# Kernel optimization log

Hardware: AMD Instinct MI355X
Metric: run time of the kernel (lower is better)

## Reference

```python
import jax, jax.numpy as jnp
import numpy as np

N, E, H, C, NG = 50000, 800000, 4, 64, 32
HC = H * C  # 256


def setup_inputs() -> dict:
    key = jax.random.key(0)
    ks = jax.random.split(key, 32)
    f32 = jnp.float32
    def rn(k, shape, s=0.1):
        return jax.random.normal(k, shape, dtype=f32) * s
    inp = {}
    inp['x'] = jax.random.normal(ks[0], (N, 4), dtype=f32)
    inp['edge_index'] = jax.random.randint(ks[1], (2, E), 0, N, dtype=jnp.int32)
    inp['edge_attr'] = jax.random.normal(ks[2], (E, 1), dtype=f32)
    inp['batch'] = jnp.sort(jax.random.randint(ks[3], (N,), 0, NG, dtype=jnp.int32))
    # encoder
    inp['enc_w'] = rn(ks[4], (4, 64)); inp['enc_b'] = rn(ks[5], (64,))
    # GATv2 layer 1: in 64 -> H*C (lin_l source, lin_r target, lin_edge, att, bias)
    inp['g1_wl'] = rn(ks[6], (64, HC)); inp['g1_bl'] = rn(ks[7], (HC,))
    inp['g1_wr'] = rn(ks[8], (64, HC)); inp['g1_br'] = rn(ks[9], (HC,))
    inp['g1_we'] = rn(ks[10], (1, HC))
    inp['g1_att'] = rn(ks[11], (H, C))
    inp['g1_bias'] = rn(ks[12], (HC,))
    # GATv2 layer 2: in 256 -> H*C
    inp['g2_wl'] = rn(ks[13], (HC, HC)); inp['g2_bl'] = rn(ks[14], (HC,))
    inp['g2_wr'] = rn(ks[15], (HC, HC)); inp['g2_br'] = rn(ks[16], (HC,))
    inp['g2_we'] = rn(ks[17], (1, HC))
    inp['g2_att'] = rn(ks[18], (H, C))
    inp['g2_bias'] = rn(ks[19], (HC,))
    # post MLP: 256 -> 128 (LayerNorm, ReLU) -> 64 (ReLU)
    inp['p1_w'] = rn(ks[20], (HC, 128)); inp['p1_b'] = rn(ks[21], (128,))
    inp['ln_g'] = jnp.ones((128,), dtype=f32); inp['ln_b'] = jnp.zeros((128,), dtype=f32)
    inp['p2_w'] = rn(ks[22], (128, 64)); inp['p2_b'] = rn(ks[23], (64,))
    return inp


def _gatv2_layer(x, src, dst, eattr, wl, bl, wr, br, we, att, bias):
    # PyG GATv2Conv: alpha_e = att . leaky_relu(lin_l(x_src) + lin_r(x_dst) + lin_edge(e))
    n = x.shape[0]
    xl = (x @ wl + bl).reshape(n, H, C)   # source-side messages
    xr = (x @ wr + br).reshape(n, H, C)   # target-side
    e = (eattr @ we).reshape(-1, H, C)
    m = jax.nn.leaky_relu(xl[src] + xr[dst] + e, 0.2)        # [E',H,C]
    alpha = jnp.einsum('ehc,hc->eh', m, att)                  # [E',H]
    amax = jax.lax.stop_gradient(jax.ops.segment_max(alpha, dst, num_segments=n))
    ex = jnp.exp(alpha - amax[dst])
    den = jax.ops.segment_sum(ex, dst, num_segments=n)
    a = ex / den[dst]                                          # softmax per dst node
    out = jax.ops.segment_sum(a[:, :, None] * xl[src], dst, num_segments=n)
    return out.reshape(n, HC) + bias


def reference(x, edge_index, edge_attr, batch, enc_w, enc_b,
              g1_wl, g1_bl, g1_wr, g1_br, g1_we, g1_att, g1_bias,
              g2_wl, g2_bl, g2_wr, g2_br, g2_we, g2_att, g2_bias,
              p1_w, p1_b, ln_g, ln_b, p2_w, p2_b):
    n = x.shape[0]
    src0, dst0 = edge_index[0], edge_index[1]
    # PyG default add_self_loops=True with fill_value='mean' for edge_attr
    deg = jnp.maximum(jax.ops.segment_sum(jnp.ones_like(edge_attr[:, 0]), dst0, num_segments=n), 1.0)
    loop_attr = jax.ops.segment_sum(edge_attr, dst0, num_segments=n) / deg[:, None]
    idx = jnp.arange(n, dtype=src0.dtype)
    src = jnp.concatenate([src0, idx]); dst = jnp.concatenate([dst0, idx])
    eattr = jnp.concatenate([edge_attr, loop_attr], axis=0)
    h = jax.nn.relu(x @ enc_w + enc_b)
    h = jax.nn.relu(_gatv2_layer(h, src, dst, eattr, g1_wl, g1_bl, g1_wr, g1_br, g1_we, g1_att, g1_bias))
    h = jax.nn.relu(_gatv2_layer(h, src, dst, eattr, g2_wl, g2_bl, g2_wr, g2_br, g2_we, g2_att, g2_bias))
    # global mean pool over graphs
    cnt = jnp.maximum(jax.ops.segment_sum(jnp.ones((n,), h.dtype), batch, num_segments=NG), 1.0)
    g = jax.ops.segment_sum(h, batch, num_segments=NG) / cnt[:, None]
    # post MLP (dropout is identity in eval)
    z = g @ p1_w + p1_b
    mu = jnp.mean(z, axis=-1, keepdims=True)
    var = jnp.mean((z - mu) ** 2, axis=-1, keepdims=True)
    z = (z - mu) / jnp.sqrt(var + 1e-5) * ln_g + ln_b
    z = jax.nn.relu(z)
    z = jax.nn.relu(z @ p2_w + p2_b)
    return z
```

## Files before the change

kernel.cpp:

```cpp
#include <hip/hip_runtime.h>

#define CDIV(a,b) (((a)+(b)-1)/(b))

typedef __bf16 bf16_t;
typedef unsigned char u8;
typedef bf16_t bf16x8 __attribute__((ext_vector_type(8)));
typedef float floatx4 __attribute__((ext_vector_type(4)));
typedef float floatx2 __attribute__((ext_vector_type(2)));

__device__ __forceinline__ int sigma2(int p) {
    int tile = p >> 7, hh = (p >> 6) & 1, m = (p >> 2) & 15, c = p & 3;
    return tile * 128 + (hh * 4 + c) * 16 + m;
}

__device__ __forceinline__ unsigned pack4_fp8(float a, float b, float c, float d) {
    int v = __builtin_amdgcn_cvt_pk_fp8_f32(a, b, 0, false);
    v = __builtin_amdgcn_cvt_pk_fp8_f32(c, d, v, true);
    return (unsigned)v;
}

template<bool HI>
__device__ __forceinline__ floatx2 cvtf8(unsigned v) {
    return __builtin_amdgcn_cvt_pk_f32_fp8(v, HI);
}

template<int CTRL>
__device__ __forceinline__ float dpp_add(float x) {
    int v = __builtin_amdgcn_update_dpp(0, __float_as_int(x), CTRL, 0xf, 0xf, true);
    return x + __int_as_float(v);
}

__global__ void k_deg(const int* __restrict__ ei, int* __restrict__ deg, int E) {
    int e = blockIdx.x * 256 + threadIdx.x;
    if (e >= E) return;
    atomicAdd(&deg[ei[E + e]], 1);
}

__global__ void k_histB(const int* __restrict__ deg, int* __restrict__ blockcnt,
                        int n, int nb) {
    __shared__ int h[64];
    int t = threadIdx.x;
    if (t < 64) h[t] = 0;
    __syncthreads();
    int i = blockIdx.x * 256 + t;
    if (i < n) {
        int d = deg[i]; if (d > 63) d = 63;
        atomicAdd(&h[63 - d], 1);
    }
    __syncthreads();
    if (t < 64) blockcnt[t * nb + blockIdx.x] = h[t];
}
__global__ void k_scan2(const int* __restrict__ bc, int* __restrict__ bo, int total) {
    __shared__ int wsum[4];
    __shared__ int carrysh;
    int t = threadIdx.x;
    int w = t >> 6, lane = t & 63;
    if (t == 0) carrysh = 0;
    __syncthreads();
    for (int base = 0; base < total; base += 256) {
        int carry = carrysh;
        int i = base + t;
        int v = (i < total) ? bc[i] : 0;
        int s = v;
        for (int d = 1; d < 64; d <<= 1) {
            int u = __shfl_up(s, d);
            if (lane >= d) s += u;
        }
        if (lane == 63) wsum[w] = s;
        __syncthreads();
        int wadd = 0;
        if (w > 0) wadd += wsum[0];
        if (w > 1) wadd += wsum[1];
        if (w > 2) wadd += wsum[2];
        if (i < total) bo[i] = carry + wadd + s - v;
        __syncthreads();
        if (t == 255) carrysh = carry + wadd + s;
        __syncthreads();
    }
}
__global__ void k_scatter2(const int* __restrict__ deg, const int* __restrict__ bo,
                           int* __restrict__ perm, int n, int nb) {
    __shared__ int h[64];
    int t = threadIdx.x;
    if (t < 64) h[t] = 0;
    __syncthreads();
    int i = blockIdx.x * 256 + t;
    int b = 0, r = 0;
    if (i < n) {
        int d = deg[i]; if (d > 63) d = 63;
        b = 63 - d;
        r = atomicAdd(&h[b], 1);
    }
    __syncthreads();
    if (i < n) perm[bo[b * nb + blockIdx.x] + r] = i;
}

__global__ void k_scanA(const int* __restrict__ deg, int* __restrict__ part, int n) {
    __shared__ int sh[256];
    int t = threadIdx.x;
    int i = blockIdx.x * 256 + t;
    int v = (i < n) ? deg[i] + 1 : 0;
    sh[t] = v;
    __syncthreads();
    for (int d = 128; d > 0; d >>= 1) { if (t < d) sh[t] += sh[t + d]; __syncthreads(); }
    if (t == 0) part[blockIdx.x] = sh[0];
}
__global__ void k_scanB(int* __restrict__ part, int nb) {
    __shared__ int sh[256];
    int t = threadIdx.x;
    int v = (t < nb) ? part[t] : 0;
    sh[t] = v;
    __syncthreads();
    for (int d = 1; d < 256; d <<= 1) {
        int u = (t >= d) ? sh[t - d] : 0;
        __syncthreads();
        sh[t] += u;
        __syncthreads();
    }
    if (t < nb) part[t] = sh[t] - v;
}
__global__ void k_scanC(const int* __restrict__ deg, const int* __restrict__ part,
                        int* __restrict__ off, int n) {
    __shared__ int sh[256];
    int t = threadIdx.x;
    int i = blockIdx.x * 256 + t;
    int v = (i < n) ? deg[i] + 1 : 0;
    sh[t] = v;
    __syncthreads();
    for (int d = 1; d < 256; d <<= 1) {
        int u = (t >= d) ? sh[t - d] : 0;
        __syncthreads();
        sh[t] += u;
        __syncthreads();
    }
    int excl = part[blockIdx.x] + sh[t] - v;
    if (i < n) off[i] = excl;
    if (i == n - 1) off[n] = excl + v;
}

__global__ void k_fill(const int* __restrict__ ei, const float* __restrict__ ea,
                       const int* __restrict__ off, int* __restrict__ cursor,
                       int2* __restrict__ csr, int E) {
    int e = blockIdx.x * 256 + threadIdx.x;
    if (e >= E) return;
    int s = ei[e], d = ei[E + e];
    int pos = off[d] + atomicAdd(&cursor[d], 1);
    csr[pos] = make_int2(s, __float_as_int(ea[e]));
}

__global__ void k_selfloop(const int* __restrict__ off, int2* __restrict__ csr, int n) {
    int i = blockIdx.x * 256 + threadIdx.x;
    if (i >= n) return;
    int p0 = off[i], p1 = off[i + 1] - 1;
    float s = 0.0f;
    for (int p = p0; p < p1; ++p) s += __int_as_float(csr[p].y);
    float la = s / fmaxf((float)(p1 - p0), 1.0f);
    csr[p1] = make_int2(i, __float_as_int(la));
}

__global__ void k_wcast2(const float* __restrict__ Wl, const float* __restrict__ Wr,
                         const float* __restrict__ bl, const float* __restrict__ br,
                         bf16_t* __restrict__ Wt, float* __restrict__ bias2,
                         int K, int kshift, int permK,
                         const float* __restrict__ we, const float* __restrict__ att,
                         const float* __restrict__ cb,
                         float* __restrict__ wep, float* __restrict__ attp,
                         float* __restrict__ cbp) {
    int idx = blockIdx.x * 256 + threadIdx.x;
    if (idx < 512) bias2[idx] = (idx < 256) ? bl[idx] : br[idx - 256];
    if (idx < 256) {
        int sg = sigma2(idx);
        wep[idx] = we[sg]; attp[idx] = att[sg]; cbp[idx] = cb[sg];
    }
    if (idx >= 512 * K) return;
    int nn = idx >> kshift, k = idx & (K - 1);
    int ks = permK ? sigma2(k) : k;
    float v = (nn < 256) ? Wl[ks * 256 + nn] : Wr[ks * 256 + (nn - 256)];
    Wt[idx] = (bf16_t)v;
}

__global__ __launch_bounds__(256) void k_gemm1_fused(
        const float* __restrict__ x, const float* __restrict__ encw,
        const float* __restrict__ encb, const bf16_t* __restrict__ Wt,
        const float* __restrict__ bias2, u8* __restrict__ XL,
        u8* __restrict__ XR, int nrows) {
    __shared__ bf16_t As[128 * 32];
    __shared__ bf16_t Bs[128 * 32];
    int tid = threadIdx.x;
    int w = tid >> 6, lane = tid & 63;
    int quad = lane >> 4, m = lane & 15;
    int row0 = blockIdx.x * 128;
    int ct0 = blockIdx.y * 2;
    bf16x8 afr[2][2];
    floatx4 acc[2][8];

    for (int ctile = ct0; ctile < ct0 + 2; ++ctile) {
        int n0 = ctile * 128;
#pragma unroll
        for (int rt = 0; rt < 2; ++rt)
#pragma unroll
            for (int ct = 0; ct < 8; ++ct)
                acc[rt][ct] = (floatx4){0.f, 0.f, 0.f, 0.f};
        for (int k0c = 0; k0c < 2; ++k0c) {
            __syncthreads();
            if (ctile == ct0) {
#pragma unroll
                for (int i = 0; i < 2; ++i) {
                    int c = tid + i * 256;
                    int r = c >> 2, kc = c & 3;
                    int sw = (kc + (r >> 1)) & 3;
                    int gr = row0 + r; if (gr >= nrows) gr = nrows - 1;
                    float4 xv = ((const float4*)x)[gr];
                    bf16x8 v;
#pragma unroll
                    for (int kk = 0; kk < 8; ++kk) {
                        int k = k0c * 32 + kc * 8 + kk;
                        float s = encb[k];
                        s = fmaf(xv.x, encw[k], s);
                        s = fmaf(xv.y, encw[64 + k], s);
                        s = fmaf(xv.z, encw[128 + k], s);
                        s = fmaf(xv.w, encw[192 + k], s);
                        v[kk] = (bf16_t)fmaxf(s, 0.0f);
                    }
                    *(bf16x8*)&As[r * 32 + sw * 8] = v;
                }
            }
#pragma unroll
            for (int i = 0; i < 2; ++i) {
                int c = tid + i * 256;
                int r = c >> 2, kc = c & 3;
                int sw = (kc + (r >> 1)) & 3;
                bf16x8 v = *(const bf16x8*)&Wt[(size_t)(n0 + r) * 64 + k0c * 32 + kc * 8];
                *(bf16x8*)&Bs[r * 32 + sw * 8] = v;
            }
            __syncthreads();
            if (ctile == ct0) {
#pragma unroll
                for (int rt = 0; rt < 2; ++rt) {
                    int ar = w * 32 + rt * 16 + m;
                    afr[k0c][rt] = *(bf16x8*)&As[ar * 32 + (((quad + (ar >> 1)) & 3) * 8)];
                }
            }
            bf16x8 bfr[8];
#pragma unroll
            for (int ct = 0; ct < 8; ++ct) {
                int br = ct * 16 + m;
                bfr[ct] = *(bf16x8*)&Bs[br * 32 + (((quad + (br >> 1)) & 3) * 8)];
            }
#pragma unroll
            for (int ct = 0; ct < 8; ++ct) {
                acc[0][ct] = __builtin_amdgcn_mfma_f32_16x16x32_bf16(afr[k0c][0], bfr[ct], acc[0][ct], 0, 0, 0);
                acc[1][ct] = __builtin_amdgcn_mfma_f32_16x16x32_bf16(afr[k0c][1], bfr[ct], acc[1][ct], 0, 0, 0);
            }
        }
        int tile = ctile & 1;
        u8* dst = (ctile < 2) ? XL : XR;
        float bv[8];
#pragma unroll
        for (int ct = 0; ct < 8; ++ct) bv[ct] = bias2[n0 + ct * 16 + m];
#pragma unroll
        for (int rt = 0; rt < 2; ++rt) {
#pragma unroll
            for (int i = 0; i < 4; ++i) {
                int row = row0 + w * 32 + rt * 16 + quad * 4 + i;
                if (row < nrows) {
                    unsigned w0 = pack4_fp8(acc[rt][0][i] + bv[0], acc[rt][1][i] + bv[1],
                                            acc[rt][2][i] + bv[2], acc[rt][3][i] + bv[3]);
                    unsigned w1 = pack4_fp8(acc[rt][4][i] + bv[4], acc[rt][5][i] + bv[5],
                                            acc[rt][6][i] + bv[6], acc[rt][7][i] + bv[7]);
                    *(unsigned*)&dst[(size_t)row * 256 + tile * 128 + m * 4] = w0;
                    *(unsigned*)&dst[(size_t)row * 256 + tile * 128 + 64 + m * 4] = w1;
                }
            }
        }
    }
}

__global__ __launch_bounds__(256) void k_gemm2(
        const bf16_t* __restrict__ Hb, const bf16_t* __restrict__ Wt,
        const float* __restrict__ bias2, u8* __restrict__ XL,
        u8* __restrict__ XR, int nrows) {
    const int K = 256;
    __shared__ bf16_t As[128 * 32];
    __shared__ bf16_t Bs[128 * 32];
    int tid = threadIdx.x;
    int w = tid >> 6, lane = tid & 63;
    int quad = lane >> 4, m = lane & 15;
    int row0 = blockIdx.x * 128;
    int ct0 = blockIdx.y * 2;
    bf16x8 afr[8][2];
    floatx4 acc[2][8];

    for (int ctile = ct0; ctile < ct0 + 2; ++ctile) {
        int n0 = ctile * 128;
#pragma unroll
        for (int rt = 0; rt < 2; ++rt)
#pragma unroll
            for (int ct = 0; ct < 8; ++ct)
                acc[rt][ct] = (floatx4){0.f, 0.f, 0.f, 0.f};
        for (int k0c = 0; k0c < 8; ++k0c) {
            __syncthreads();
            if (ctile == ct0) {
#pragma unroll
                for (int i = 0; i < 2; ++i) {
                    int c = tid + i * 256;
                    int r = c >> 2, kc = c & 3;
                    int sw = (kc + (r >> 1)) & 3;
                    int gr = row0 + r; if (gr >= nrows) gr = nrows - 1;
                    bf16x8 v = *(const bf16x8*)&Hb[(size_t)gr * K + k0c * 32 + kc * 8];
                    *(bf16x8*)&As[r * 32 + sw * 8] = v;
                }
            }
#pragma unroll
            for (int i = 0; i < 2; ++i) {
                int c = tid + i * 256;
                int r = c >> 2, kc = c & 3;
                int sw = (kc + (r >> 1)) & 3;
                bf16x8 v = *(const bf16x8*)&Wt[(size_t)(n0 + r) * K + k0c * 32 + kc * 8];
                *(bf16x8*)&Bs[r * 32 + sw * 8] = v;
            }
            __syncthreads();
            if (ctile == ct0) {
#pragma unroll
                for (int rt = 0; rt < 2; ++rt) {
                    int ar = w * 32 + rt * 16 + m;
                    afr[k0c][rt] = *(bf16x8*)&As[ar * 32 + (((quad + (ar >> 1)) & 3) * 8)];
                }
            }
            bf16x8 bfr[8];
#pragma unroll
            for (int ct = 0; ct < 8; ++ct) {
                int br = ct * 16 + m;
                bfr[ct] = *(bf16x8*)&Bs[br * 32 + (((quad + (br >> 1)) & 3) * 8)];
            }
#pragma unroll
            for (int ct = 0; ct < 8; ++ct) {
                acc[0][ct] = __builtin_amdgcn_mfma_f32_16x16x32_bf16(afr[k0c][0], bfr[ct], acc[0][ct], 0, 0, 0);
                acc[1][ct] = __builtin_amdgcn_mfma_f32_16x16x32_bf16(afr[k0c][1], bfr[ct], acc[1][ct], 0, 0, 0);
            }
        }
        int tile = ctile & 1;
        u8* dst = (ctile < 2) ? XL : XR;
        float bv[8];
#pragma unroll
        for (int ct = 0; ct < 8; ++ct) bv[ct] = bias2[n0 + ct * 16 + m];
#pragma unroll
        for (int rt = 0; rt < 2; ++rt) {
#pragma unroll
            for (int i = 0; i < 4; ++i) {
                int row = row0 + w * 32 + rt * 16 + quad * 4 + i;
                if (row < nrows) {
                    unsigned w0 = pack4_fp8(acc[rt][0][i] + bv[0], acc[rt][1][i] + bv[1],
                                            acc[rt][2][i] + bv[2], acc[rt][3][i] + bv[3]);
                    unsigned w1 = pack4_fp8(acc[rt][4][i] + bv[4], acc[rt][5][i] + bv[5],
                                            acc[rt][6][i] + bv[6], acc[rt][7][i] + bv[7]);
                    *(unsigned*)&dst[(size_t)row * 256 + tile * 128 + m * 4] = w0;
                    *(unsigned*)&dst[(size_t)row * 256 + tile * 128 + 64 + m * 4] = w1;
                }
            }
        }
    }
}

__global__ void k_conv(
                       const u8* __restrict__ XL, const u8* __restrict__ XR,
                       const float* __restrict__ wep, const float* __restrict__ attp,
                       const int2* __restrict__ csr,
                       const int* __restrict__ off, const float* __restrict__ cbp,
                       const int* __restrict__ perm,
                       bf16_t* __restrict__ outb, int n) {
    int wid = (blockIdx.x * 256 + threadIdx.x) >> 6;
    int lane = threadIdx.x & 63;
    if (wid >= n) return;
    int node = perm[wid];
    int l = lane & 31, half = lane >> 5;
    int loff = l * 8;
    uint2 ur = *(const uint2*)(XR + (size_t)node * 256 + loff);
    floatx2 xr01 = cvtf8<false>(ur.x);
    floatx2 xr23 = cvtf8<true>(ur.x);
    floatx2 xr45 = cvtf8<false>(ur.y);
    floatx2 xr67 = cvtf8<true>(ur.y);
    float4 wa = ((const float4*)wep)[2 * l], wb = ((const float4*)wep)[2 * l + 1];
    float4 aa = ((const float4*)attp)[2 * l], ab = ((const float4*)attp)[2 * l + 1];
    floatx2 wv01 = {wa.x, wa.y}, wv23 = {wa.z, wa.w};
    floatx2 wv45 = {wb.x, wb.y}, wv67 = {wb.z, wb.w};
    const float LOG2E = 1.44269504f;
    floatx2 av01 = {aa.x * LOG2E, aa.y * LOG2E}, av23 = {aa.z * LOG2E, aa.w * LOG2E};
    floatx2 av45 = {ab.x * LOG2E, ab.y * LOG2E}, av67 = {ab.z * LOG2E, ab.w * LOG2E};
    int p0 = off[node], p1 = off[node + 1];
    float s = 0.f;
    floatx2 a01 = {0.f, 0.f}, a23 = {0.f, 0.f}, a45 = {0.f, 0.f}, a67 = {0.f, 0.f};

    for (int base = p0; base < p1; base += 64) {
        int rem = p1 - base;
        int cnt = (rem < 64) ? rem : 64;
        int gp = base + lane; if (gp > p1 - 1) gp = p1 - 1;
        int2 ed = csr[gp];

        auto fetch = [&](int j, uint2& u, float& ev) {
            int sl = j + half; if (sl >= cnt) sl = cnt - 1;
            int sx = __shfl(ed.x, sl);
            ev = __int_as_float(__shfl(ed.y, sl));
            u = *(const uint2*)(XL + (unsigned)(sx * 256 + loff));
        };

        uint2 u0, u1, u2; float e0, e1, e2;
        fetch(0, u0, e0);
        fetch(2, u1, e1);
        fetch(4, u2, e2);

#pragma unroll 3
        for (int j = 0; j < cnt; j += 2) {
            uint2 un; float en;
            fetch(j + 6, un, en);
            floatx2 x01 = cvtf8<false>(u0.x);
            floatx2 x23 = cvtf8<true>(u0.x);
            floatx2 x45 = cvtf8<false>(u0.y);
            floatx2 x67 = cvtf8<true>(u0.y);
            floatx2 t01 = x01 + xr01 + e0 * wv01;
            floatx2 t23 = x23 + xr23 + e0 * wv23;
            floatx2 t45 = x45 + xr45 + e0 * wv45;
            floatx2 t67 = x67 + xr67 + e0 * wv67;
            t01 = __builtin_elementwise_max(t01, 0.2f * t01);
            t23 = __builtin_elementwise_max(t23, 0.2f * t23);
            t45 = __builtin_elementwise_max(t45, 0.2f * t45);
            t67 = __builtin_elementwise_max(t67, 0.2f * t67);
            floatx2 d = t01 * av01 + t23 * av23 + t45 * av45 + t67 * av67;
            float al = d.x + d.y;
            al = dpp_add<0xB1>(al);
            al = dpp_add<0x4E>(al);
            al = dpp_add<0x141>(al);
            float wg = (j + half < cnt) ? exp2f(al) : 0.0f;
            s += wg;
            a01 += wg * x01; a23 += wg * x23; a45 += wg * x45; a67 += wg * x67;
            u0 = u1; e0 = e1; u1 = u2; e1 = e2; u2 = un; e2 = en;
        }
    }

    s += __shfl_xor(s, 32);
    a01.x += __shfl_xor(a01.x, 32); a01.y += __shfl_xor(a01.y, 32);
    a23.x += __shfl_xor(a23.x, 32); a23.y += __shfl_xor(a23.y, 32);
    a45.x += __shfl_xor(a45.x, 32); a45.y += __shfl_xor(a45.y, 32);
    a67.x += __shfl_xor(a67.x, 32); a67.y += __shfl_xor(a67.y, 32);
    if (half == 0) {
        float inv = 1.0f / s;
        float4 ba = ((const float4*)cbp)[2 * l], bb = ((const float4*)cbp)[2 * l + 1];
        bf16x8 ob;
        ob[0] = (bf16_t)fmaxf(fmaf(a01.x, inv, ba.x), 0.f);
        ob[1] = (bf16_t)fmaxf(fmaf(a01.y, inv, ba.y), 0.f);
        ob[2] = (bf16_t)fmaxf(fmaf(a23.x, inv, ba.z), 0.f);
        ob[3] = (bf16_t)fmaxf(fmaf(a23.y, inv, ba.w), 0.f);
        ob[4] = (bf16_t)fmaxf(fmaf(a45.x, inv, bb.x), 0.f);
        ob[5] = (bf16_t)fmaxf(fmaf(a45.y, inv, bb.y), 0.f);
        ob[6] = (bf16_t)fmaxf(fmaf(a67.x, inv, bb.z), 0.f);
        ob[7] = (bf16_t)fmaxf(fmaf(a67.y, inv, bb.w), 0.f);
        *(bf16x8*)&outb[(size_t)node * 256 + l * 8] = ob;
    }
}

__global__ void k_pool(const bf16_t* __restrict__ h, const int* __restrict__ batch,
                       float* __restrict__ gsum, float* __restrict__ gcnt, int n) {
    int j = threadIdx.x;
    int start = blockIdx.x * 32;
    if (start >= n) return;
    int end = start + 32; if (end > n) end = n;
    int cur = batch[start];
    float acc = 0.0f, cnt = 0.0f;
    for (int i = start; i < end; ++i) {
        int g = batch[i];
        if (g != cur) {
            atomicAdd(&gsum[cur * 256 + j], acc);
            if (j == 0) atomicAdd(&gcnt[cur], cnt);
            acc = 0.0f; cnt = 0.0f; cur = g;
        }
        acc += (float)h[(size_t)i * 256 + j];
        cnt += 1.0f;
    }
    atomicAdd(&gsum[cur * 256 + j], acc);
    if (j == 0) atomicAdd(&gcnt[cur], cnt);
}

__global__ void k_mlp(const float* __restrict__ gsum, const float* __restrict__ gcnt,
                      const float* __restrict__ p1w, const float* __restrict__ p1b,
                      const float* __restrict__ lng, const float* __restrict__ lnb,
                      const float* __restrict__ p2w, const float* __restrict__ p2b,
                      float* __restrict__ out) {
    int g = blockIdx.x;
    int t = threadIdx.x;
    __shared__ float gv[256];
    __shared__ float z[128];
    __shared__ float red[128];
    float invc = 1.0f / fmaxf(gcnt[g], 1.0f);
    gv[sigma2(t)]       = gsum[g * 256 + t] * invc;
    gv[sigma2(t + 128)] = gsum[g * 256 + 128 + t] * invc;
    __syncthreads();
    float z1 = p1b[t];
    for (int k = 0; k < 256; ++k) z1 = fmaf(gv[k], p1w[k * 128 + t], z1);
    red[t] = z1;
    __syncthreads();
    for (int d = 64; d > 0; d >>= 1) { if (t < d) red[t] += red[t + d]; __syncthreads(); }
    float mu = red[0] * (1.0f / 128.0f);
    __syncthreads();
    float dz = z1 - mu;
    red[t] = dz * dz;
    __syncthreads();
    for (int d = 64; d > 0; d >>= 1) { if (t < d) red[t] += red[t + d]; __syncthreads(); }
    float var = red[0] * (1.0f / 128.0f);
    float zn = dz * rsqrtf(var + 1e-5f) * lng[t] + lnb[t];
    z[t] = fmaxf(zn, 0.0f);
    __syncthreads();
    if (t < 64) {
        float o = p2b[t];
        for (int k = 0; k < 128; ++k) o = fmaf(z[k], p2w[k * 64 + t], o);
        out[g * 64 + t] = fmaxf(o, 0.0f);
    }
}

extern "C" void kernel_launch(void* const* d_in, const int* in_sizes, int n_in,
                              void* d_out, int out_size, void* d_ws, size_t ws_size,
                              hipStream_t stream) {
    const float* x      = (const float*)d_in[0];
    const int*   ei     = (const int*)d_in[1];
    const float* ea     = (const float*)d_in[2];
    const int*   batch  = (const int*)d_in[3];
    const float* enc_w  = (const float*)d_in[4];
    const float* enc_b  = (const float*)d_in[5];
    const float* g1_wl  = (const float*)d_in[6];
    const float* g1_bl  = (const float*)d_in[7];
    const float* g1_wr  = (const float*)d_in[8];
    const float* g1_br  = (const float*)d_in[9];
    const float* g1_we  = (const float*)d_in[10];
    const float* g1_att = (const float*)d_in[11];
    const float* g1_bias= (const float*)d_in[12];
    const float* g2_wl  = (const float*)d_in[13];
    const float* g2_bl  = (const float*)d_in[14];
    const float* g2_wr  = (const float*)d_in[15];
    const float* g2_br  = (const float*)d_in[16];
    const float* g2_we  = (const float*)d_in[17];
    const float* g2_att = (const float*)d_in[18];
    const float* g2_bias= (const float*)d_in[19];
    const float* p1_w   = (const float*)d_in[20];
    const float* p1_b   = (const float*)d_in[21];
    const float* ln_g   = (const float*)d_in[22];
    const float* ln_b   = (const float*)d_in[23];
    const float* p2_w   = (const float*)d_in[24];
    const float* p2_b   = (const float*)d_in[25];
    float* out = (float*)d_out;

    const int N  = in_sizes[3];
    const int E  = in_sizes[1] / 2;
    const int EE = E + N;
    const int NB = CDIV(N, 256);

    u8*     XL  = (u8*)d_ws;
    u8*     XR  = XL + (size_t)N * 256;
    bf16_t* Hb  = (bf16_t*)(XR + (size_t)N * 256);
    bf16_t* Wt  = Hb + (size_t)N * 256;
    int2*  csr  = (int2*)(Wt + 512 * 256);
    float* gsum  = (float*)(csr + EE);
    float* gcnt  = gsum + 32 * 256;
    int*   deg   = (int*)(gcnt + 32);
    int*   cursor= deg + N;
    float* bias2 = (float*)(cursor + N);
    float* wep   = bias2 + 512;
    float* attp  = wep + 256;
    float* cbp   = attp + 256;
    int*   part  = (int*)(cbp + 256);
    int*   off   = part + 256;
    int*   perm  = off + (N + 1);
    int*   blockcnt = perm + N;
    int*   blockoff = blockcnt + 64 * NB;

    (void)hipMemsetAsync(gsum, 0, (size_t)(2 * N + 32 * 256 + 32) * sizeof(float), stream);

    k_deg<<<CDIV(E, 256), 256, 0, stream>>>(ei, deg, E);
    k_histB<<<NB, 256, 0, stream>>>(deg, blockcnt, N, NB);
    k_scan2<<<1, 256, 0, stream>>>(blockcnt, blockoff, 64 * NB);
    k_scatter2<<<NB, 256, 0, stream>>>(deg, blockoff, perm, N, NB);

    k_scanA<<<NB, 256, 0, stream>>>(deg, part, N);
    k_scanB<<<1, 256, 0, stream>>>(part, NB);
    k_scanC<<<NB, 256, 0, stream>>>(deg, part, off, N);
    k_fill<<<CDIV(E, 256), 256, 0, stream>>>(ei, ea, off, cursor, csr, E);
    k_selfloop<<<NB, 256, 0, stream>>>(off, csr, N);

    dim3 ggrid(CDIV(N, 128), 2);

    k_wcast2<<<CDIV(512 * 64, 256), 256, 0, stream>>>(g1_wl, g1_wr, g1_bl, g1_br, Wt, bias2,
                                                      64, 6, 0, g1_we, g1_att, g1_bias,
                                                      wep, attp, cbp);
    k_gemm1_fused<<<ggrid, 256, 0, stream>>>(x, enc_w, enc_b, Wt, bias2, XL, XR, N);
    k_conv<<<CDIV(N, 4), 256, 0, stream>>>(XL, XR, wep, attp, csr, off, cbp, perm, Hb, N);

    k_wcast2<<<CDIV(512 * 256, 256), 256, 0, stream>>>(g2_wl, g2_wr, g2_bl, g2_br, Wt, bias2,
                                                       256, 8, 1, g2_we, g2_att, g2_bias,
                                                       wep, attp, cbp);
    k_gemm2<<<ggrid, 256, 0, stream>>>(Hb, Wt, bias2, XL, XR, N);
    k_conv<<<CDIV(N, 4), 256, 0, stream>>>(XL, XR, wep, attp, csr, off, cbp, perm, Hb, N);

    k_pool<<<CDIV(N, 32), 256, 0, stream>>>(Hb, batch, gsum, gcnt, N);
    k_mlp<<<32, 128, 0, stream>>>(gsum, gcnt, p1_w, p1_b, ln_g, ln_b, p2_w, p2_b, out);
}
```

Baseline: 459.1 us.

## Handle self-loops inside conv and parallelize bucket scan with merged preprocessing

Removes the explicit self-loop slot from the CSR and the k_selfloop kernel. The conv kernel now computes the mean edge attribute with a wave reduction and processes the self-loop term directly from the node's own XL row. The serial single-block bucket scan is replaced by a multi-block reduce/scan/apply scheme, and the histogram is fused into the degree partial-sum kernel. LeakyReLU is rewritten as 0.6*x + 0.4*|x| folded into the attention weights. This removes a sequential scan and an extra pass over the CSR, at the cost of more ALU work per edge in the conv loop.

Result: faster. 428.1 us (-6.8%).

```diff
diff --git a/kernel.cpp b/kernel.cpp
--- a/kernel.cpp
+++ b/kernel.cpp
@@ -36,47 +36,93 @@
     atomicAdd(&deg[ei[E + e]], 1);
 }
 
-__global__ void k_histB(const int* __restrict__ deg, int* __restrict__ blockcnt,
-                        int n, int nb) {
+__global__ void k_scanA(const int* __restrict__ deg, int* __restrict__ part,
+                        int* __restrict__ blockcnt, int n, int nb) {
+    __shared__ int sh[256];
     __shared__ int h[64];
     int t = threadIdx.x;
     if (t < 64) h[t] = 0;
-    __syncthreads();
     int i = blockIdx.x * 256 + t;
+    int v = (i < n) ? deg[i] : 0;
+    __syncthreads();
     if (i < n) {
-        int d = deg[i]; if (d > 63) d = 63;
+        int d = v > 63 ? 63 : v;
         atomicAdd(&h[63 - d], 1);
     }
-    __syncthreads();
+    sh[t] = v;
+    __syncthreads();
+    for (int d = 128; d > 0; d >>= 1) { if (t < d) sh[t] += sh[t + d]; __syncthreads(); }
+    if (t == 0) part[blockIdx.x] = sh[0];
     if (t < 64) blockcnt[t * nb + blockIdx.x] = h[t];
 }
-__global__ void k_scan2(const int* __restrict__ bc, int* __restrict__ bo, int total) {
-    __shared__ int wsum[4];
-    __shared__ int carrysh;
+__global__ void k_bucketA(const int* __restrict__ bc, int* __restrict__ bpart, int total) {
+    __shared__ int sh[256];
     int t = threadIdx.x;
-    int w = t >> 6, lane = t & 63;
-    if (t == 0) carrysh = 0;
-    __syncthreads();
-    for (int base = 0; base < total; base += 256) {
-        int carry = carrysh;
-        int i = base + t;
-        int v = (i < total) ? bc[i] : 0;
-        int s = v;
-        for (int d = 1; d < 64; d <<= 1) {
-            int u = __shfl_up(s, d);
-            if (lane >= d) s += u;
-        }
-        if (lane == 63) wsum[w] = s;
-        __syncthreads();
-        int wadd = 0;
-        if (w > 0) wadd += wsum[0];
-        if (w > 1) wadd += wsum[1];
-        if (w > 2) wadd += wsum[2];
-        if (i < total) bo[i] = carry + wadd + s - v;
-        __syncthreads();
-        if (t == 255) carrysh = carry + wadd + s;
-        __syncthreads();
-    }
+    int i = blockIdx.x * 256 + t;
+    sh[t] = (i < total) ? bc[i] : 0;
+    __syncthreads();
+    for (int d = 128; d > 0; d >>= 1) { if (t < d) sh[t] += sh[t + d]; __syncthreads(); }
+    if (t == 0) bpart[blockIdx.x] = sh[0];
+}
+__global__ void k_scanB2(int* __restrict__ part, int nb,
+                         int* __restrict__ bpart, int nbb) {
+    __shared__ int sh[256];
+    int t = threadIdx.x;
+    int v = (t < nb) ? part[t] : 0;
+    sh[t] = v;
+    __syncthreads();
+    for (int d = 1; d < 256; d <<= 1) {
+        int u = (t >= d) ? sh[t - d] : 0;
+        __syncthreads();
+        sh[t] += u;
+        __syncthreads();
+    }
+    if (t < nb) part[t] = sh[t] - v;
+    __syncthreads();
+    int v2 = (t < nbb) ? bpart[t] : 0;
+    sh[t] = v2;
+    __syncthreads();
+    for (int d = 1; d < 256; d <<= 1) {
+        int u = (t >= d) ? sh[t - d] : 0;
+        __syncthreads();
+        sh[t] += u;
+        __syncthreads();
+    }
+    if (t < nbb) bpart[t] = sh[t] - v2;
+}
+__global__ void k_scanC(const int* __restrict__ deg, const int* __restrict__ part,
+                        int* __restrict__ off, int n) {
+    __shared__ int sh[256];
+    int t = threadIdx.x;
+    int i = blockIdx.x * 256 + t;
+    int v = (i < n) ? deg[i] : 0;
+    sh[t] = v;
+    __syncthreads();
+    for (int d = 1; d < 256; d <<= 1) {
+        int u = (t >= d) ? sh[t - d] : 0;
+        __syncthreads();
+        sh[t] += u;
+        __syncthreads();
+    }
+    int excl = part[blockIdx.x] + sh[t] - v;
+    if (i < n) off[i] = excl;
+    if (i == n - 1) off[n] = excl + v;
+}
+__global__ void k_bucketC(const int* __restrict__ bc, const int* __restrict__ bpart,
+                          int* __restrict__ bo, int total) {
+    __shared__ int sh[256];
+    int t = threadIdx.x;
+    int i = blockIdx.x * 256 + t;
+    int v = (i < total) ? bc[i] : 0;
+    sh[t] = v;
+    __syncthreads();
+    for (int d = 1; d < 256; d <<= 1) {
+        int u = (t >= d) ? sh[t - d] : 0;
+        __syncthreads();
+        sh[t] += u;
+        __syncthreads();
+    }
+    if (i < total) bo[i] = bpart[blockIdx.x] + sh[t] - v;
 }
 __global__ void k_scatter2(const int* __restrict__ deg, const int* __restrict__ bo,
                            int* __restrict__ perm, int n, int nb) {
@@ -93,49 +139,6 @@
     }
     __syncthreads();
     if (i < n) perm[bo[b * nb + blockIdx.x] + r] = i;
-}
-
-__global__ void k_scanA(const int* __restrict__ deg, int* __restrict__ part, int n) {
-    __shared__ int sh[256];
-    int t = threadIdx.x;
-    int i = blockIdx.x * 256 + t;
-    int v = (i < n) ? deg[i] + 1 : 0;
-    sh[t] = v;
-    __syncthreads();
-    for (int d = 128; d > 0; d >>= 1) { if (t < d) sh[t] += sh[t + d]; __syncthreads(); }
-    if (t == 0) part[blockIdx.x] = sh[0];
-}
-__global__ void k_scanB(int* __restrict__ part, int nb) {
-    __shared__ int sh[256];
-    int t = threadIdx.x;
-    int v = (t < nb) ? part[t] : 0;
-    sh[t] = v;
-    __syncthreads();
-    for (int d = 1; d < 256; d <<= 1) {
-        int u = (t >= d) ? sh[t - d] : 0;
-        __syncthreads();
-        sh[t] += u;
-        __syncthreads();
-    }
-    if (t < nb) part[t] = sh[t] - v;
-}
-__global__ void k_scanC(const int* __restrict__ deg, const int* __restrict__ part,
-                        int* __restrict__ off, int n) {
-    __shared__ int sh[256];
-    int t = threadIdx.x;
-    int i = blockIdx.x * 256 + t;
-    int v = (i < n) ? deg[i] + 1 : 0;
-    sh[t] = v;
-    __syncthreads();
-    for (int d = 1; d < 256; d <<= 1) {
-        int u = (t >= d) ? sh[t - d] : 0;
-        __syncthreads();
-        sh[t] += u;
-        __syncthreads();
-    }
-    int excl = part[blockIdx.x] + sh[t] - v;
-    if (i < n) off[i] = excl;
-    if (i == n - 1) off[n] = excl + v;
 }
 
 __global__ void k_fill(const int* __restrict__ ei, const float* __restrict__ ea,
@@ -146,16 +149,6 @@
     int s = ei[e], d = ei[E + e];
     int pos = off[d] + atomicAdd(&cursor[d], 1);
     csr[pos] = make_int2(s, __float_as_int(ea[e]));
-}
-
-__global__ void k_selfloop(const int* __restrict__ off, int2* __restrict__ csr, int n) {
-    int i = blockIdx.x * 256 + threadIdx.x;
-    if (i >= n) return;
-    int p0 = off[i], p1 = off[i + 1] - 1;
-    float s = 0.0f;
-    for (int p = p0; p < p1; ++p) s += __int_as_float(csr[p].y);
-    float la = s / fmaxf((float)(p1 - p0), 1.0f);
-    csr[p1] = make_int2(i, __float_as_int(la));
 }
 
 __global__ void k_wcast2(const float* __restrict__ Wl, const float* __restrict__ Wr,
@@ -376,6 +369,7 @@
     int l = lane & 31, half = lane >> 5;
     int loff = l * 8;
     uint2 ur = *(const uint2*)(XR + (size_t)node * 256 + loff);
+    uint2 us = *(const uint2*)(XL + (size_t)node * 256 + loff);
     floatx2 xr01 = cvtf8<false>(ur.x);
     floatx2 xr23 = cvtf8<true>(ur.x);
     floatx2 xr45 = cvtf8<false>(ur.y);
@@ -384,11 +378,11 @@
     float4 aa = ((const float4*)attp)[2 * l], ab = ((const float4*)attp)[2 * l + 1];
     floatx2 wv01 = {wa.x, wa.y}, wv23 = {wa.z, wa.w};
     floatx2 wv45 = {wb.x, wb.y}, wv67 = {wb.z, wb.w};
-    const float LOG2E = 1.44269504f;
-    floatx2 av01 = {aa.x * LOG2E, aa.y * LOG2E}, av23 = {aa.z * LOG2E, aa.w * LOG2E};
-    floatx2 av45 = {ab.x * LOG2E, ab.y * LOG2E}, av67 = {ab.z * LOG2E, ab.w * LOG2E};
+    const float C6 = 0.6f * 1.44269504f;
+    floatx2 av01 = {aa.x * C6, aa.y * C6}, av23 = {aa.z * C6, aa.w * C6};
+    floatx2 av45 = {ab.x * C6, ab.y * C6}, av67 = {ab.z * C6, ab.w * C6};
     int p0 = off[node], p1 = off[node + 1];
-    float s = 0.f;
+    float s = 0.f, sea = 0.f;
     floatx2 a01 = {0.f, 0.f}, a23 = {0.f, 0.f}, a45 = {0.f, 0.f}, a67 = {0.f, 0.f};
 
     for (int base = p0; base < p1; base += 64) {
@@ -397,10 +391,16 @@
         int gp = base + lane; if (gp > p1 - 1) gp = p1 - 1;
         int2 ed = csr[gp];
 
-        auto fetch = [&](int j, uint2& u, float& ev) {
+        float ev = (lane < cnt) ? __int_as_float(ed.y) : 0.f;
+        ev += __shfl_xor(ev, 1);  ev += __shfl_xor(ev, 2);
+        ev += __shfl_xor(ev, 4);  ev += __shfl_xor(ev, 8);
+        ev += __shfl_xor(ev, 16); ev += __shfl_xor(ev, 32);
+        sea += ev;
+
+        auto fetch = [&](int j, uint2& u, float& e) {
             int sl = j + half; if (sl >= cnt) sl = cnt - 1;
             int sx = __shfl(ed.x, sl);
-            ev = __int_as_float(__shfl(ed.y, sl));
+            e = __int_as_float(__shfl(ed.y, sl));
             u = *(const uint2*)(XL + (unsigned)(sx * 256 + loff));
         };
 
@@ -421,12 +421,16 @@
             floatx2 t23 = x23 + xr23 + e0 * wv23;
             floatx2 t45 = x45 + xr45 + e0 * wv45;
             floatx2 t67 = x67 + xr67 + e0 * wv67;
-            t01 = __builtin_elementwise_max(t01, 0.2f * t01);
-            t23 = __builtin_elementwise_max(t23, 0.2f * t23);
-            t45 = __builtin_elementwise_max(t45, 0.2f * t45);
-            t67 = __builtin_elementwise_max(t67, 0.2f * t67);
-            floatx2 d = t01 * av01 + t23 * av23 + t45 * av45 + t67 * av67;
-            float al = d.x + d.y;
+            floatx2 d6 = t01 * av01 + t23 * av23 + t45 * av45 + t67 * av67;
+            float db =      av01.x * fabsf(t01.x);
+            db = fmaf(av01.y, fabsf(t01.y), db);
+            db = fmaf(av23.x, fabsf(t23.x), db);
+            db = fmaf(av23.y, fabsf(t23.y), db);
+            db = fmaf(av45.x, fabsf(t45.x), db);
+            db = fmaf(av45.y, fabsf(t45.y), db);
+            db = fmaf(av67.x, fabsf(t67.x), db);
+            db = fmaf(av67.y, fabsf(t67.y), db);
+            float al = fmaf(0.66666667f, db, d6.x + d6.y);
             al = dpp_add<0xB1>(al);
             al = dpp_add<0x4E>(al);
             al = dpp_add<0x141>(al);
@@ -442,6 +446,36 @@
     a23.x += __shfl_xor(a23.x, 32); a23.y += __shfl_xor(a23.y, 32);
     a45.x += __shfl_xor(a45.x, 32); a45.y += __shfl_xor(a45.y, 32);
     a67.x += __shfl_xor(a67.x, 32); a67.y += __shfl_xor(a67.y, 32);
+
+    {
+        float dg = (float)(p1 - p0);
+        float la = sea / fmaxf(dg, 1.0f);
+        floatx2 xs01 = cvtf8<false>(us.x);
+        floatx2 xs23 = cvtf8<true>(us.x);
+        floatx2 xs45 = cvtf8<false>(us.y);
+        floatx2 xs67 = cvtf8<true>(us.y);
+        floatx2 t01 = xs01 + xr01 + la * wv01;
+        floatx2 t23 = xs23 + xr23 + la * wv23;
+        floatx2 t45 = xs45 + xr45 + la * wv45;
+        floatx2 t67 = xs67 + xr67 + la * wv67;
+        floatx2 d6 = t01 * av01 + t23 * av23 + t45 * av45 + t67 * av67;
+        float db =      av01.x * fabsf(t01.x);
+        db = fmaf(av01.y, fabsf(t01.y), db);
+        db = fmaf(av23.x, fabsf(t23.x), db);
+        db = fmaf(av23.y, fabsf(t23.y), db);
+        db = fmaf(av45.x, fabsf(t45.x), db);
+        db = fmaf(av45.y, fabsf(t45.y), db);
+        db = fmaf(av67.x, fabsf(t67.x), db);
+        db = fmaf(av67.y, fabsf(t67.y), db);
+        float al = fmaf(0.66666667f, db, d6.x + d6.y);
+        al = dpp_add<0xB1>(al);
+        al = dpp_add<0x4E>(al);
+        al = dpp_add<0x141>(al);
+        float wg = exp2f(al);
+        s += wg;
+        a01 += wg * xs01; a23 += wg * xs23; a45 += wg * xs45; a67 += wg * xs67;
+    }
+
     if (half == 0) {
         float inv = 1.0f / s;
         float4 ba = ((const float4*)cbp)[2 * l], bb = ((const float4*)cbp)[2 * l + 1];
@@ -551,6 +585,8 @@
     const int E  = in_sizes[1] / 2;
     const int EE = E + N;
     const int NB = CDIV(N, 256);
+    const int NBT = 64 * NB;
+    const int NBB = CDIV(NBT, 256);
 
     u8*     XL  = (u8*)d_ws;
     u8*     XR  = XL + (size_t)N * 256;
@@ -569,20 +605,19 @@
     int*   off   = part + 256;
     int*   perm  = off + (N + 1);
     int*   blockcnt = perm + N;
-    int*   blockoff = blockcnt + 64 * NB;
+    int*   blockoff = blockcnt + NBT;
+    int*   bpart    = blockoff + NBT;
 
     (void)hipMemsetAsync(gsum, 0, (size_t)(2 * N + 32 * 256 + 32) * sizeof(float), stream);
 
     k_deg<<<CDIV(E, 256), 256, 0, stream>>>(ei, deg, E);
-    k_histB<<<NB, 256, 0, stream>>>(deg, blockcnt, N, NB);
-    k_scan2<<<1, 256, 0, stream>>>(blockcnt, blockoff, 64 * NB);
+    k_scanA<<<NB, 256, 0, stream>>>(deg, part, blockcnt, N, NB);
+    k_bucketA<<<NBB, 256, 0, stream>>>(blockcnt, bpart, NBT);
+    k_scanB2<<<1, 256, 0, stream>>>(part, NB, bpart, NBB);
+    k_scanC<<<NB, 256, 0, stream>>>(deg, part, off, N);
+    k_bucketC<<<NBB, 256, 0, stream>>>(blockcnt, bpart, blockoff, NBT);
     k_scatter2<<<NB, 256, 0, stream>>>(deg, blockoff, perm, N, NB);
-
-    k_scanA<<<NB, 256, 0, stream>>>(deg, part, N);
-    k_scanB<<<1, 256, 0, stream>>>(part, NB);
-    k_scanC<<<NB, 256, 0, stream>>>(deg, part, off, N);
     k_fill<<<CDIV(E, 256), 256, 0, stream>>>(ei, ea, off, cursor, csr, E);
-    k_selfloop<<<NB, 256, 0, stream>>>(off, csr, N);
 
     dim3 ggrid(CDIV(N, 128), 2);
 
```
